# Kernel optimization log

Hardware: AMD Instinct MI355X
Metric: run time of the kernel (lower is better)

Reference implementation:

```python
import jax, jax.numpy as jnp
import numpy as np

B, A, S, T, DE, D3 = 8, 32, 16, 750, 25, 58
L, DZ = 4, 512
KL_P = 0.0002


def setup_inputs() -> dict:
    key = jax.random.key(0)
    ks = jax.random.split(key, 6)
    return {
        "gt_emotion": jax.random.normal(ks[0], (B * A, T, DE), jnp.float32),
        "gt_3dmm": jax.random.normal(ks[1], (B * A, T, D3), jnp.float32),
        "pred_emotion": jax.random.normal(ks[2], (B * S, T, DE), jnp.float32),
        "pred_3dmm": jax.random.normal(ks[3], (B * S, T, D3), jnp.float32),
        "dist_mu": jax.random.normal(ks[4], (L, B * S, DZ), jnp.float32),
        "dist_scale": jax.random.uniform(ks[5], (L, B * S, DZ), jnp.float32, 0.5, 1.5),
        "num_appropriate": jnp.full((B,), A, jnp.int32),
        "num_samples": jnp.full((B,), S, jnp.int32),
    }


def reference(gt_emotion, gt_3dmm, pred_emotion, pred_3dmm, dist_mu, dist_scale,
              num_appropriate, num_samples):
    b = num_appropriate.shape[0]
    a = gt_emotion.shape[0] // b      # appropriate reactions per batch element
    s = pred_emotion.shape[0] // b    # predicted samples per batch element
    t, de = gt_emotion.shape[1], gt_emotion.shape[2]
    d3 = gt_3dmm.shape[2]

    ge = gt_emotion.reshape(b, a, t, de)
    g3 = gt_3dmm.reshape(b, a, t, d3)
    pe = pred_emotion.reshape(b, s, t, de)
    p3 = pred_3dmm.reshape(b, s, t, d3)

    # pairwise mean-MSE cost between every pred sample and every appropriate gt
    ce = jnp.mean((pe[:, :, None] - ge[:, None]) ** 2, axis=(3, 4))                    # [b,s,a]
    c1 = jnp.mean((p3[:, :, None, :, :52] - g3[:, None, :, :, :52]) ** 2, axis=(3, 4))
    c2 = jnp.mean((p3[:, :, None, :, 52:] - g3[:, None, :, :, 52:]) ** 2, axis=(3, 4))
    cost = ce + c1 + 10.0 * c2

    idx = jnp.argmin(cost, axis=2)                     # [b,s] best-match index (torch.no_grad)
    bidx = jnp.arange(b)[:, None]
    ge_sel = ge[bidx, idx]                             # [b,s,t,de] gathered gt
    g3_sel = g3[bidx, idx]                             # [b,s,t,d3]

    rec_loss = (jnp.mean((pe - ge_sel) ** 2)
                + jnp.mean((p3[..., :52] - g3_sel[..., :52]) ** 2)
                + 10.0 * jnp.mean((p3[..., 52:] - g3_sel[..., 52:]) ** 2))

    # KL(N(mu, scale) || N(0, 1)), mean per layer then averaged over layers
    kl = -jnp.log(dist_scale) + 0.5 * (dist_scale ** 2 + dist_mu ** 2 - 1.0)
    kld_loss = jnp.mean(kl)

    loss = rec_loss + KL_P * kld_loss
    return (loss, rec_loss, kld_loss)
```

## Files before the change

### kernel.cpp

```cpp
#include <hip/hip_runtime.h>

#define NB 8
#define NA 32
#define NS 16
#define NT 750
#define NDE 25
#define ND3 58
#define KE (NT * NDE)
#define K3 (NT * ND3)
#define NL 4
#define NDZ 512
#define NKL (NL * NB * NS * NDZ)

#define POS_PER_B 8
#define SLABS 16
#define SE_SLABS 5
#define SE_CHUNK 3750
#define S3_CHUNK 3955
#define COST_BLOCKS (NB * POS_PER_B * SLABS)
#define KL_BLOCKS 64
#define KL_PER_THR (NKL / (KL_BLOCKS * 256))

#define SW_E  0.0073029674f
#define SW_1  0.0050637127f
#define SW_2  0.0471404521f

__device__ __forceinline__ void tile_step(
    const float* __restrict__ srcP, const float* __restrict__ srcG,
    int K, int k, float sw, float acc[64])
{
    float p[8], g[8];
    #pragma unroll
    for (int i = 0; i < 8; ++i) p[i] = srcP[i * K + k] * sw;
    #pragma unroll
    for (int j = 0; j < 8; ++j) g[j] = srcG[j * K + k] * sw;
    #pragma unroll
    for (int i = 0; i < 8; ++i)
        #pragma unroll
        for (int j = 0; j < 8; ++j) {
            const float d = p[i] - g[j];
            acc[i * 8 + j] = fmaf(d, d, acc[i * 8 + j]);
        }
}

__global__ __launch_bounds__(256) void fused_kernel(
    const float* __restrict__ ge, const float* __restrict__ g3,
    const float* __restrict__ pe, const float* __restrict__ p3,
    const float* __restrict__ mu, const float* __restrict__ sc,
    float* __restrict__ wsCost, float* __restrict__ wsKL)
{
    const int blk = blockIdx.x;
    const int tid = threadIdx.x;
    __shared__ float red[4][64];

    if (blk >= COST_BLOCKS) {
        const int kb = blk - COST_BLOCKS;
        float ks = 0.f;
        #pragma unroll
        for (int it = 0; it < KL_PER_THR; ++it) {
            const int i = kb * (256 * KL_PER_THR) + it * 256 + tid;
            const float m = mu[i], sg = sc[i];
            ks += 0.5f * (sg * sg + m * m - 1.0f) - logf(sg);
        }
        #pragma unroll
        for (int o = 32; o > 0; o >>= 1) ks += __shfl_xor(ks, o);
        const int lane = tid & 63, w = tid >> 6;
        if (lane == 0) red[0][w] = ks;
        __syncthreads();
        if (tid == 0) wsKL[kb] = red[0][0] + red[0][1] + red[0][2] + red[0][3];
        return;
    }

    const int b    = blk / (POS_PER_B * SLABS);
    const int rem  = blk % (POS_PER_B * SLABS);
    const int pos  = rem / SLABS;
    const int slab = rem % SLABS;
    const int s0   = (pos >> 2) * 8;
    const int a0   = (pos & 3) * 8;

    const bool isE = slab < SE_SLABS;
    const int  K   = isE ? KE : K3;
    const int  k0  = isE ? slab * SE_CHUNK : (slab - SE_SLABS) * S3_CHUNK;
    const int  kend = isE ? k0 + SE_CHUNK : min(k0 + S3_CHUNK, K3);

    const float* __restrict__ srcP = isE ? pe + (size_t)(b * NS + s0) * KE
                                         : p3 + (size_t)(b * NS + s0) * K3;
    const float* __restrict__ srcG = isE ? ge + (size_t)(b * NA + a0) * KE
                                         : g3 + (size_t)(b * NA + a0) * K3;

    float acc[64];
    #pragma unroll
    for (int i = 0; i < 64; ++i) acc[i] = 0.f;

    if (isE) {
        for (int k = k0 + tid; k < kend; k += 256)
            tile_step(srcP, srcG, K, k, SW_E, acc);
    } else {
        int col = (k0 + tid) % ND3;
        for (int k = k0 + tid; k < kend; k += 256) {
            const float sw = (col < 52) ? SW_1 : SW_2;
            tile_step(srcP, srcG, K, k, sw, acc);
            col += 256 % ND3;
            if (col >= ND3) col -= ND3;
        }
    }

    const int lane = tid & 63;
    int n = 64;
    #pragma unroll
    for (int step = 0; step < 6; ++step) {
        const int o = 1 << step;
        const bool hi = (lane & o) != 0;
        const int h = n >> 1;
        #pragma unroll
        for (int m = 0; m < h; ++m) {
            const float send = hi ? acc[m] : acc[m + h];
            const float recv = __shfl_xor(send, o);
            acc[m] = (hi ? acc[m + h] : acc[m]) + recv;
        }
        n = h;
    }

    const int w = tid >> 6;
    red[w][__brev((unsigned)lane) >> 26] = acc[0];
    __syncthreads();
    if (tid < 64)
        wsCost[blk * 64 + tid] = red[0][tid] + red[1][tid] + red[2][tid] + red[3][tid];
}

__global__ __launch_bounds__(1024) void finalize_kernel(
    const float* __restrict__ wsCost, const float* __restrict__ wsKL,
    float* __restrict__ out)
{
    const int t = threadIdx.x;
    const int b  = t >> 7;
    const int s  = (t >> 3) & 15;
    const int a4 = t & 7;
    const int ptile = s >> 3, irow = s & 7;

    float mn = 1e30f;
    #pragma unroll
    for (int q = 0; q < 4; ++q) {
        const int a   = a4 * 4 + q;
        const int pos = ptile * 4 + (a >> 3);
        const int j   = a & 7;
        const float* src = wsCost + ((b * POS_PER_B + pos) * SLABS) * 64 + irow * 8 + j;
        float sum = 0.f;
        #pragma unroll
        for (int slab = 0; slab < SLABS; ++slab) sum += src[slab * 64];
        mn = fminf(mn, sum);
    }
    mn = fminf(mn, __shfl_xor(mn, 1));
    mn = fminf(mn, __shfl_xor(mn, 2));
    mn = fminf(mn, __shfl_xor(mn, 4));

    float contrib = ((t & 7) == 0) ? mn : 0.f;
    #pragma unroll
    for (int o = 32; o > 0; o >>= 1) contrib += __shfl_xor(contrib, o);

    __shared__ float r2[16];
    if ((t & 63) == 0) r2[t >> 6] = contrib;

    float kl = (t < 64) ? wsKL[t] : 0.f;
    #pragma unroll
    for (int o = 32; o > 0; o >>= 1) kl += __shfl_xor(kl, o);

    __syncthreads();
    if (t == 0) {
        float rec = 0.f;
        #pragma unroll
        for (int w = 0; w < 16; ++w) rec += r2[w];
        rec *= (1.0f / (NB * NS));
        const float kld = kl * (1.0f / (float)NKL);
        out[0] = fmaf(0.0002f, kld, rec);
        out[1] = rec;
        out[2] = kld;
    }
}

extern "C" void kernel_launch(void* const* d_in, const int* in_sizes, int n_in,
                              void* d_out, int out_size, void* d_ws, size_t ws_size,
                              hipStream_t stream)
{
    const float* ge = (const float*)d_in[0];
    const float* g3 = (const float*)d_in[1];
    const float* pe = (const float*)d_in[2];
    const float* p3 = (const float*)d_in[3];
    const float* mu = (const float*)d_in[4];
    const float* sc = (const float*)d_in[5];

    float* wsCost = (float*)d_ws;
    float* wsKL   = wsCost + COST_BLOCKS * 64;

    fused_kernel<<<COST_BLOCKS + KL_BLOCKS, 256, 0, stream>>>(
        ge, g3, pe, p3, mu, sc, wsCost, wsKL);
    finalize_kernel<<<1, 1024, 0, stream>>>(wsCost, wsKL, (float*)d_out);
}
```

Baseline: 178.7 us.

## Vectorize cost tile loads to float2, double slabs, reduce via atomics

The pairwise cost tiles now load float2 pairs instead of scalars, and the K dimension is split into 32 slabs instead of 16, doubling the block count. Launch bounds request 4 blocks per CU. Partial costs and the KL sum are accumulated with atomicAdd into a compact cost matrix zeroed by a memset, so the finalize kernel only takes row minima. The aim is better memory throughput and occupancy and a cheaper final reduction, at the cost of an extra memset launch, atomic contention and non-deterministic summation order. The 3DMM column weighting is now chosen per float2 pair, which relies on the 52/58 split falling on even boundaries.

After: 156.4 us. 1.14x faster.

```diff
diff --git a/kernel.cpp b/kernel.cpp
--- a/kernel.cpp
+++ b/kernel.cpp
@@ -3,20 +3,17 @@
 #define NB 8
 #define NA 32
 #define NS 16
-#define NT 750
-#define NDE 25
+#define KE 18750
+#define K3 43500
 #define ND3 58
-#define KE (NT * NDE)
-#define K3 (NT * ND3)
-#define NL 4
-#define NDZ 512
-#define NKL (NL * NB * NS * NDZ)
+#define NKL 262144
 
 #define POS_PER_B 8
-#define SLABS 16
-#define SE_SLABS 5
-#define SE_CHUNK 3750
-#define S3_CHUNK 3955
+#define SE_SLABS 10
+#define S3_SLABS 22
+#define SLABS 32
+#define CH_E 1876
+#define CH_3 1978
 #define COST_BLOCKS (NB * POS_PER_B * SLABS)
 #define KL_BLOCKS 64
 #define KL_PER_THR (NKL / (KL_BLOCKS * 256))
@@ -25,29 +22,11 @@
 #define SW_1  0.0050637127f
 #define SW_2  0.0471404521f
 
-__device__ __forceinline__ void tile_step(
-    const float* __restrict__ srcP, const float* __restrict__ srcG,
-    int K, int k, float sw, float acc[64])
-{
-    float p[8], g[8];
-    #pragma unroll
-    for (int i = 0; i < 8; ++i) p[i] = srcP[i * K + k] * sw;
-    #pragma unroll
-    for (int j = 0; j < 8; ++j) g[j] = srcG[j * K + k] * sw;
-    #pragma unroll
-    for (int i = 0; i < 8; ++i)
-        #pragma unroll
-        for (int j = 0; j < 8; ++j) {
-            const float d = p[i] - g[j];
-            acc[i * 8 + j] = fmaf(d, d, acc[i * 8 + j]);
-        }
-}
-
-__global__ __launch_bounds__(256) void fused_kernel(
+__global__ __launch_bounds__(256, 4) void fused_kernel(
     const float* __restrict__ ge, const float* __restrict__ g3,
     const float* __restrict__ pe, const float* __restrict__ p3,
     const float* __restrict__ mu, const float* __restrict__ sc,
-    float* __restrict__ wsCost, float* __restrict__ wsKL)
+    float* __restrict__ cost, float* __restrict__ klsum)
 {
     const int blk = blockIdx.x;
     const int tid = threadIdx.x;
@@ -67,41 +46,77 @@
         const int lane = tid & 63, w = tid >> 6;
         if (lane == 0) red[0][w] = ks;
         __syncthreads();
-        if (tid == 0) wsKL[kb] = red[0][0] + red[0][1] + red[0][2] + red[0][3];
+        if (tid == 0)
+            atomicAdd(klsum, red[0][0] + red[0][1] + red[0][2] + red[0][3]);
         return;
     }
 
-    const int b    = blk / (POS_PER_B * SLABS);
-    const int rem  = blk % (POS_PER_B * SLABS);
-    const int pos  = rem / SLABS;
-    const int slab = rem % SLABS;
+    const int b    = blk >> 8;
+    const int rem  = blk & 255;
+    const int pos  = rem >> 5;
+    const int slab = rem & 31;
     const int s0   = (pos >> 2) * 8;
     const int a0   = (pos & 3) * 8;
 
     const bool isE = slab < SE_SLABS;
-    const int  K   = isE ? KE : K3;
-    const int  k0  = isE ? slab * SE_CHUNK : (slab - SE_SLABS) * S3_CHUNK;
-    const int  kend = isE ? k0 + SE_CHUNK : min(k0 + S3_CHUNK, K3);
+    const int  KH  = (isE ? KE : K3) >> 1;
+    const int  c0  = isE ? slab * CH_E : (slab - SE_SLABS) * CH_3;
+    const int  kk0 = (c0 >> 1) + tid;
+    const int  kkend = min((c0 + (isE ? CH_E : CH_3)) >> 1, KH);
 
-    const float* __restrict__ srcP = isE ? pe + (size_t)(b * NS + s0) * KE
-                                         : p3 + (size_t)(b * NS + s0) * K3;
-    const float* __restrict__ srcG = isE ? ge + (size_t)(b * NA + a0) * KE
-                                         : g3 + (size_t)(b * NA + a0) * K3;
+    const float2* __restrict__ P = (const float2*)(isE ? pe + (size_t)(b * NS + s0) * KE
+                                                       : p3 + (size_t)(b * NS + s0) * K3);
+    const float2* __restrict__ G = (const float2*)(isE ? ge + (size_t)(b * NA + a0) * KE
+                                                       : g3 + (size_t)(b * NA + a0) * K3);
 
     float acc[64];
     #pragma unroll
     for (int i = 0; i < 64; ++i) acc[i] = 0.f;
 
     if (isE) {
-        for (int k = k0 + tid; k < kend; k += 256)
-            tile_step(srcP, srcG, K, k, SW_E, acc);
+        for (int kk = kk0; kk < kkend; kk += 256) {
+            float2 p[8], g[8];
+            #pragma unroll
+            for (int i = 0; i < 8; ++i) { p[i] = P[i * KH + kk]; }
+            #pragma unroll
+            for (int j = 0; j < 8; ++j) { g[j] = G[j * KH + kk]; }
+            #pragma unroll
+            for (int i = 0; i < 8; ++i) { p[i].x *= SW_E; p[i].y *= SW_E; }
+            #pragma unroll
+            for (int j = 0; j < 8; ++j) { g[j].x *= SW_E; g[j].y *= SW_E; }
+            #pragma unroll
+            for (int i = 0; i < 8; ++i)
+                #pragma unroll
+                for (int j = 0; j < 8; ++j) {
+                    const float d0 = p[i].x - g[j].x;
+                    const float d1 = p[i].y - g[j].y;
+                    float t = fmaf(d0, d0, acc[i * 8 + j]);
+                    acc[i * 8 + j] = fmaf(d1, d1, t);
+                }
+        }
     } else {
-        int col = (k0 + tid) % ND3;
-        for (int k = k0 + tid; k < kend; k += 256) {
+        int col = (2 * kk0) % ND3;
+        for (int kk = kk0; kk < kkend; kk += 256) {
             const float sw = (col < 52) ? SW_1 : SW_2;
-            tile_step(srcP, srcG, K, k, sw, acc);
-            col += 256 % ND3;
-            if (col >= ND3) col -= ND3;
+            col += 48; if (col >= ND3) col -= ND3;
+            float2 p[8], g[8];
+            #pragma unroll
+            for (int i = 0; i < 8; ++i) { p[i] = P[i * KH + kk]; }
+            #pragma unroll
+            for (int j = 0; j < 8; ++j) { g[j] = G[j * KH + kk]; }
+            #pragma unroll
+            for (int i = 0; i < 8; ++i) { p[i].x *= sw; p[i].y *= sw; }
+            #pragma unroll
+            for (int j = 0; j < 8; ++j) { g[j].x *= sw; g[j].y *= sw; }
+            #pragma unroll
+            for (int i = 0; i < 8; ++i)
+                #pragma unroll
+                for (int j = 0; j < 8; ++j) {
+                    const float d0 = p[i].x - g[j].x;
+                    const float d1 = p[i].y - g[j].y;
+                    float t = fmaf(d0, d0, acc[i * 8 + j]);
+                    acc[i * 8 + j] = fmaf(d1, d1, t);
+                }
         }
     }
 
@@ -124,54 +139,33 @@
     const int w = tid >> 6;
     red[w][__brev((unsigned)lane) >> 26] = acc[0];
     __syncthreads();
-    if (tid < 64)
-        wsCost[blk * 64 + tid] = red[0][tid] + red[1][tid] + red[2][tid] + red[3][tid];
+    if (tid < 64) {
+        const float v = red[0][tid] + red[1][tid] + red[2][tid] + red[3][tid];
+        const int i = tid >> 3, j = tid & 7;
+        atomicAdd(&cost[b * (NS * NA) + (s0 + i) * NA + (a0 + j)], v);
+    }
 }
 
-__global__ __launch_bounds__(1024) void finalize_kernel(
-    const float* __restrict__ wsCost, const float* __restrict__ wsKL,
+__global__ __launch_bounds__(128) void finalize_kernel(
+    const float* __restrict__ cost, const float* __restrict__ klsum,
     float* __restrict__ out)
 {
     const int t = threadIdx.x;
-    const int b  = t >> 7;
-    const int s  = (t >> 3) & 15;
-    const int a4 = t & 7;
-    const int ptile = s >> 3, irow = s & 7;
-
+    const float4* row = (const float4*)(cost + t * NA);
     float mn = 1e30f;
     #pragma unroll
-    for (int q = 0; q < 4; ++q) {
-        const int a   = a4 * 4 + q;
-        const int pos = ptile * 4 + (a >> 3);
-        const int j   = a & 7;
-        const float* src = wsCost + ((b * POS_PER_B + pos) * SLABS) * 64 + irow * 8 + j;
-        float sum = 0.f;
-        #pragma unroll
-        for (int slab = 0; slab < SLABS; ++slab) sum += src[slab * 64];
-        mn = fminf(mn, sum);
+    for (int q = 0; q < 8; ++q) {
+        const float4 v = row[q];
+        mn = fminf(mn, fminf(fminf(v.x, v.y), fminf(v.z, v.w)));
     }
-    mn = fminf(mn, __shfl_xor(mn, 1));
-    mn = fminf(mn, __shfl_xor(mn, 2));
-    mn = fminf(mn, __shfl_xor(mn, 4));
-
-    float contrib = ((t & 7) == 0) ? mn : 0.f;
     #pragma unroll
-    for (int o = 32; o > 0; o >>= 1) contrib += __shfl_xor(contrib, o);
-
-    __shared__ float r2[16];
-    if ((t & 63) == 0) r2[t >> 6] = contrib;
-
-    float kl = (t < 64) ? wsKL[t] : 0.f;
-    #pragma unroll
-    for (int o = 32; o > 0; o >>= 1) kl += __shfl_xor(kl, o);
-
+    for (int o = 32; o > 0; o >>= 1) mn += __shfl_xor(mn, o);
+    __shared__ float r2[2];
+    if ((t & 63) == 0) r2[t >> 6] = mn;
     __syncthreads();
     if (t == 0) {
-        float rec = 0.f;
-        #pragma unroll
-        for (int w = 0; w < 16; ++w) rec += r2[w];
-        rec *= (1.0f / (NB * NS));
-        const float kld = kl * (1.0f / (float)NKL);
+        const float rec = (r2[0] + r2[1]) * (1.0f / (NB * NS));
+        const float kld = klsum[0] * (1.0f / (float)NKL);
         out[0] = fmaf(0.0002f, kld, rec);
         out[1] = rec;
         out[2] = kld;
@@ -189,10 +183,12 @@
     const float* mu = (const float*)d_in[4];
     const float* sc = (const float*)d_in[5];
 
-    float* wsCost = (float*)d_ws;
-    float* wsKL   = wsCost + COST_BLOCKS * 64;
+    float* cost  = (float*)d_ws;
+    float* klsum = cost + NB * NS * NA;
+
+    hipMemsetAsync(d_ws, 0, (NB * NS * NA + 1) * sizeof(float), stream);
 
     fused_kernel<<<COST_BLOCKS + KL_BLOCKS, 256, 0, stream>>>(
-        ge, g3, pe, p3, mu, sc, wsCost, wsKL);
-    finalize_kernel<<<1, 1024, 0, stream>>>(wsCost, wsKL, (float*)d_out);
+        ge, g3, pe, p3, mu, sc, cost, klsum);
+    finalize_kernel<<<1, 128, 0, stream>>>(cost, klsum, (float*)d_out);
 }
```
